# Kernel optimization log

Measured on AMD Instinct MI355X. Metric: run time of the kernel, lower is better.

Reference implementation:

```python
import jax, jax.numpy as jnp
import numpy as np

VOCAB = 32000   # vocab size
EDIM = 1024     # embedding dim
HDIM = 1024     # encoder hidden dim (fhid dim)
NACTS = 2       # ACTS = {'push': 0, 'pop': 1}
NCLASSES = 3
L = 256         # len_total
B = 128         # bsz
PAD = 0         # padding_idx
PUSH, POP = 0, 1


def setup_inputs() -> dict:
    key = jax.random.key(0)
    ks = jax.random.split(key, 10)

    def mk_seq(kt, kl):
        tok = jax.random.randint(kt, (L, B), 1, VOCAB)          # non-pad tokens
        lens = jax.random.randint(kl, (B,), L // 2, L - 1)      # ragged lengths
        t = jnp.arange(L)[:, None]
        # first lens+1 positions non-pad (so lens = L - n_pad - 1 as in the module)
        return jnp.where(t < lens[None, :] + 1, tok, PAD)

    seq1 = mk_seq(ks[0], ks[1])
    seq2 = mk_seq(ks[2], ks[3])

    def w(k, shp):
        return (jax.random.normal(k, shp, jnp.float32) * 0.02)

    return {
        "seq1": seq1, "seq2": seq2,
        "emb": w(ks[4], (VOCAB, EDIM)),
        "W_top": w(ks[5], (EDIM, HDIM)), "b_top": jnp.zeros((HDIM,), jnp.float32),
        "W_act": w(ks[6], (EDIM, NACTS)), "b_act": jnp.zeros((NACTS,), jnp.float32),
        "W1": w(ks[7], (4 * HDIM, HDIM)), "b1": jnp.zeros((HDIM,), jnp.float32),
        "W2": w(ks[8], (HDIM, NCLASSES)), "b2": jnp.zeros((NCLASSES,), jnp.float32),
    }


def _encode(seq, emb, W_top, b_top, W_act, b_act):
    # stub stack-encoder: time dim 2L-1 (one shift + one reduce step per token)
    seq_ext = jnp.concatenate([seq, seq[:-1]], axis=0)          # [2L-1, B]
    x = emb[seq_ext]                                            # [2L-1, B, E]
    top = jnp.tanh(jnp.einsum('tbe,eh->tbh', x, W_top) + b_top) # [2L-1, B, H]
    act = jax.nn.softmax(jnp.einsum('tbe,ea->tba', x, W_act) + b_act, axis=-1)
    return top, act


def _ragged_stats(act, Ts, bsz):
    # masked equivalents of the per-sample python loops over acts[:T, b, :]
    Tmax = act.shape[0]
    mask = (jnp.arange(Tmax)[:, None] < Ts[None, :]).astype(act.dtype)  # [2L-1, B]
    Tf = Ts.astype(act.dtype)
    push, pop = act[:, :, PUSH], act[:, :, POP]
    sum_push = (push * mask).sum(axis=0) / Tf                   # [B]
    sum_pop = ((pop * mask).sum(axis=0) + 1.0) / Tf             # [B]
    diff = jnp.sqrt((((push - pop) ** 2) * mask).sum(axis=0)) / Tf  # [B]
    dis = jnp.linalg.norm(sum_push - sum_pop) / bsz             # scalar
    return dis, diff.sum() / bsz


def reference(seq1, seq2, emb, W_top, b_top, W_act, b_act, W1, b1, W2, b2):
    bsz = seq1.shape[1]
    top1, act1 = _encode(seq1, emb, W_top, b_top, W_act, b_act)
    top2, act2 = _encode(seq2, emb, W_top, b_top, W_act, b_act)

    lens1 = seq1.shape[0] - (seq1 == PAD).sum(axis=0) - 1
    lens2 = seq2.shape[0] - (seq2 == PAD).sum(axis=0) - 1
    Ts1 = 2 * lens1 - 1
    Ts2 = 2 * lens2 - 1

    barange = jnp.arange(bsz)
    fhid1 = top1[Ts1 - 1, barange]                              # [B, H] ragged gather
    fhid2 = top2[Ts2 - 1, barange]

    u = jnp.concatenate([fhid1, fhid2, jnp.abs(fhid1 - fhid2), fhid1 * fhid2], axis=-1)
    res_clf = jax.nn.relu(u @ W1 + b1) @ W2 + b2                # [B, nclasses]

    dis1, diff1 = _ragged_stats(act1, Ts1, bsz)
    dis2, diff2 = _ragged_stats(act2, Ts2, bsz)
    return (res_clf, dis1, dis2, diff1, diff2)
```

## Files before the change

kernel.cpp:

```cpp
#include <hip/hip_runtime.h>
#include <math.h>

#define LL 256
#define BB 128
#define EDIM 1024
#define HDIM 1024
#define VOCAB 32000

#define NKSF 8
#define NKS  64

#define WS_EACT   0
#define WS_DELTA  32000
#define WS_DIFFB  32256
#define WS_FHID   33024
#define WS_BIG    295168

#define APAD 68

__device__ __forceinline__ void fma4(float4& a, float s, const float4& w) {
  a.x = fmaf(s, w.x, a.x); a.y = fmaf(s, w.y, a.y);
  a.z = fmaf(s, w.z, a.z); a.w = fmaf(s, w.w, a.w);
}

extern "C" __global__ __launch_bounds__(256)
void k_fh_eact(const float* __restrict__ emb, const float* __restrict__ Wtop,
               const float* __restrict__ Wact,
               const int* __restrict__ seq1, const int* __restrict__ seq2,
               float* __restrict__ fpart, float* __restrict__ Eact) {
  __shared__ float ash[128 * APAD];
  __shared__ int stok[128];
  int blk = blockIdx.x, tid = threadIdx.x;
  if (blk >= 256) {
    int lane = tid & 63, wave = tid >> 6;
    int v = (blk - 256) * 4 + wave;
    const float4* row = (const float4*)(emb + (size_t)v * EDIM);
    const float4* w4 = (const float4*)Wact;
    float a0 = 0.f;
#pragma unroll
    for (int it = 0; it < 4; ++it) {
      int i = lane + it * 64;
      float4 x = row[i];
      float4 wa = w4[2 * i];
      float4 wb = w4[2 * i + 1];
      a0 = fmaf(x.x, wa.x - wa.y, a0);
      a0 = fmaf(x.y, wa.z - wa.w, a0);
      a0 = fmaf(x.z, wb.x - wb.y, a0);
      a0 = fmaf(x.w, wb.z - wb.w, a0);
    }
#pragma unroll
    for (int off = 32; off; off >>= 1)
      a0 += __shfl_down(a0, off, 64);
    if (lane == 0) Eact[v] = a0;
    return;
  }
  int ks = blk >> 5, rb = (blk >> 4) & 1, cb = blk & 15;
  int cg = tid & 15, rgr = tid >> 4;
  int c0 = cb * 64 + cg * 4;
  int kbase = ks * 128;
  const int* seq = rb ? seq2 : seq1;
  {
    int c = tid >> 1, h = tid & 1;
    int z = 0;
    int base = h * 128;
    for (int r = 0; r < 128; ++r)
      z += (seq[(base + r) * BB + c] == 0) ? 1 : 0;
    z += __shfl_xor(z, 1, 64);
    if (h == 0) {
      int lens = 255 - z;
      int tt = 2 * lens - 2;
      int idx = (tt < LL) ? tt : tt - LL;
      stok[c] = seq[idx * BB + c];
    }
  }
  float4 acc[8];
#pragma unroll
  for (int r = 0; r < 8; ++r) acc[r] = make_float4(0.f, 0.f, 0.f, 0.f);
#pragma unroll
  for (int ch = 0; ch < 2; ++ch) {
    int kg = kbase + ch * 64;
    __syncthreads();
    for (int idx = tid; idx < 128 * 16; idx += 256) {
      int r = idx >> 4, q = idx & 15;
      *(float4*)&ash[r * APAD + q * 4] =
          ((const float4*)(emb + (size_t)stok[r] * EDIM + kg))[q];
    }
    __syncthreads();
    const float* Wp = Wtop + (size_t)kg * HDIM + c0;
    float4 w[4];
#pragma unroll
    for (int j = 0; j < 4; ++j) w[j] = *(const float4*)(Wp + (size_t)j * HDIM);
#pragma unroll
    for (int kk = 0; kk < 64; kk += 4) {
      float4 wn[4];
      if (kk + 4 < 64) {
#pragma unroll
        for (int j = 0; j < 4; ++j) wn[j] = *(const float4*)(Wp + (size_t)(kk + 4 + j) * HDIM);
      }
#pragma unroll
      for (int r = 0; r < 8; ++r) {
        float4 a = *(const float4*)&ash[(rgr * 8 + r) * APAD + kk];
        fma4(acc[r], a.x, w[0]); fma4(acc[r], a.y, w[1]);
        fma4(acc[r], a.z, w[2]); fma4(acc[r], a.w, w[3]);
      }
#pragma unroll
      for (int j = 0; j < 4; ++j) w[j] = wn[j];
    }
  }
  float* dst = fpart + ((size_t)ks * 256 + rb * 128 + rgr * 8) * HDIM + c0;
#pragma unroll
  for (int r = 0; r < 8; ++r)
    *(float4*)(dst + (size_t)r * HDIM) = acc[r];
}

extern "C" __global__ __launch_bounds__(256)
void k_ftanh_stats(const float* __restrict__ fpart, const float* __restrict__ btop,
                   const int* __restrict__ seq1, const int* __restrict__ seq2,
                   const float* __restrict__ Eact, const float* __restrict__ b_act,
                   float* __restrict__ fhid, float* __restrict__ delta,
                   float* __restrict__ diffb) {
  int blk = blockIdx.x, tid = threadIdx.x;
  if (blk < 256) {
    int g = blk * 256 + tid;
    float4 s = ((const float4*)fpart)[g];
#pragma unroll
    for (int k = 1; k < NKSF; ++k) {
      float4 p = ((const float4*)fpart)[(size_t)k * 65536 + g];
      s.x += p.x; s.y += p.y; s.z += p.z; s.w += p.w;
    }
    float4 b = ((const float4*)btop)[g & 255];
    ((float4*)fhid)[g] = make_float4(tanhf(s.x + b.x), tanhf(s.y + b.y),
                                     tanhf(s.z + b.z), tanhf(s.w + b.w));
    return;
  }
  int sb = blk - 256;
  int s = sb >> 7, b = sb & 127;
  const int* seq = s ? seq2 : seq1;
  __shared__ int col[LL];
  __shared__ int zred[256];
  __shared__ float redf[256];
  int v = seq[tid * BB + b];
  col[tid] = v;
  zred[tid] = (v == 0) ? 1 : 0;
  __syncthreads();
  for (int off = 128; off; off >>= 1) {
    if (tid < off) zred[tid] += zred[tid + off];
    __syncthreads();
  }
  int lens = LL - zred[0] - 1;
  int Ts = 2 * lens - 1;
  float ba = b_act[0] - b_act[1];
  float sp = 0.f, sq = 0.f;
  for (int t = tid; t < Ts; t += 256) {
    int tok = (t < LL) ? col[t] : col[t - LL];
    float d = Eact[tok] + ba;
    float p0 = 1.0f / (1.0f + expf(-d));
    float dd = 2.f * p0 - 1.f;
    sp += dd;
    sq = fmaf(dd, dd, sq);
  }
  redf[tid] = sp; __syncthreads();
  for (int off = 128; off; off >>= 1) { if (tid < off) redf[tid] += redf[tid + off]; __syncthreads(); }
  float tsp = redf[0]; __syncthreads();
  redf[tid] = sq; __syncthreads();
  for (int off = 128; off; off >>= 1) { if (tid < off) redf[tid] += redf[tid + off]; __syncthreads(); }
  if (tid == 0) {
    float Tf = (float)Ts;
    delta[sb] = (tsp - 1.0f) / Tf;
    diffb[sb] = sqrtf(redf[0]) / Tf;
  }
}

extern "C" __global__ __launch_bounds__(256)
void k_part(const float* __restrict__ fhid, const float* __restrict__ W1,
            float* __restrict__ part) {
  __shared__ float ush[128 * APAD];
  int blk = blockIdx.x, tid = threadIdx.x;
  int ksb = blk >> 4, cb = blk & 15;
  int cg = tid & 15, rgr = tid >> 4;
  int c0 = cb * 64 + cg * 4;
  int kbase = ksb * 64;
  int seg = kbase >> 10;
  int fb4 = (kbase & 1023) >> 2;
  const float4* f4 = (const float4*)fhid;
#pragma unroll
  for (int j = 0; j < 8; ++j) {
    int idx = tid + j * 256;
    int r = idx >> 4, q = idx & 15;
    float4 u;
    if (seg == 0) u = f4[r * 256 + fb4 + q];
    else if (seg == 1) u = f4[(128 + r) * 256 + fb4 + q];
    else {
      float4 f1 = f4[r * 256 + fb4 + q];
      float4 f2 = f4[(128 + r) * 256 + fb4 + q];
      if (seg == 2)
        u = make_float4(fabsf(f1.x - f2.x), fabsf(f1.y - f2.y),
                        fabsf(f1.z - f2.z), fabsf(f1.w - f2.w));
      else
        u = make_float4(f1.x * f2.x, f1.y * f2.y, f1.z * f2.z, f1.w * f2.w);
    }
    *(float4*)&ush[r * APAD + q * 4] = u;
  }
  float4 acc[8];
#pragma unroll
  for (int r = 0; r < 8; ++r) acc[r] = make_float4(0.f, 0.f, 0.f, 0.f);
  __syncthreads();
  const float* Wp = W1 + (size_t)kbase * HDIM + c0;
  float4 w[4];
#pragma unroll
  for (int j = 0; j < 4; ++j) w[j] = *(const float4*)(Wp + (size_t)j * HDIM);
#pragma unroll
  for (int kk = 0; kk < 64; kk += 4) {
    float4 wn[4];
    if (kk + 4 < 64) {
#pragma unroll
      for (int j = 0; j < 4; ++j) wn[j] = *(const float4*)(Wp + (size_t)(kk + 4 + j) * HDIM);
    }
#pragma unroll
    for (int r = 0; r < 8; ++r) {
      float4 a = *(const float4*)&ush[(rgr * 8 + r) * APAD + kk];
      fma4(acc[r], a.x, w[0]); fma4(acc[r], a.y, w[1]);
      fma4(acc[r], a.z, w[2]); fma4(acc[r], a.w, w[3]);
    }
#pragma unroll
    for (int j = 0; j < 4; ++j) w[j] = wn[j];
  }
  float* dst = part + ((size_t)ksb * 128 + rgr * 8) * HDIM + c0;
#pragma unroll
  for (int r = 0; r < 8; ++r)
    *(float4*)(dst + (size_t)r * HDIM) = acc[r];
}

extern "C" __global__ __launch_bounds__(256)
void k_clf_final(const float* __restrict__ part, const float* __restrict__ b1,
                 const float* __restrict__ W2, const float* __restrict__ b2,
                 const float* __restrict__ delta, const float* __restrict__ diffb,
                 float* __restrict__ out) {
  int blk = blockIdx.x, tid = threadIdx.x;
  __shared__ float red[768];
  if (blk == 128) {
    for (int s = 0; s < 2; ++s) {
      float v = 0.f, w = 0.f;
      if (tid < BB) { float d = delta[s * BB + tid]; v = d * d; w = diffb[s * BB + tid]; }
      red[tid] = v; __syncthreads();
      for (int off = 128; off; off >>= 1) { if (tid < off) red[tid] += red[tid + off]; __syncthreads(); }
      if (tid == 0) out[384 + s] = sqrtf(red[0]) / (float)BB;
      __syncthreads();
      red[tid] = w; __syncthreads();
      for (int off = 128; off; off >>= 1) { if (tid < off) red[tid] += red[tid + off]; __syncthreads(); }
      if (tid == 0) out[386 + s] = red[0] / (float)BB;
      __syncthreads();
    }
    return;
  }
  int b = blk;
  float4 p = ((const float4*)b1)[tid];
  const float4* p4 = (const float4*)part;
  for (int ks = 0; ks < NKS; ++ks) {
    float4 q = p4[((size_t)ks * 128 + b) * 256 + tid];
    p.x += q.x; p.y += q.y; p.z += q.z; p.w += q.w;
  }
  p.x = fmaxf(p.x, 0.f); p.y = fmaxf(p.y, 0.f);
  p.z = fmaxf(p.z, 0.f); p.w = fmaxf(p.w, 0.f);
  int k0 = tid * 4;
  float a0 = 0.f, a1 = 0.f, a2 = 0.f;
  a0 = fmaf(p.x, W2[(k0 + 0) * 3 + 0], a0); a1 = fmaf(p.x, W2[(k0 + 0) * 3 + 1], a1); a2 = fmaf(p.x, W2[(k0 + 0) * 3 + 2], a2);
  a0 = fmaf(p.y, W2[(k0 + 1) * 3 + 0], a0); a1 = fmaf(p.y, W2[(k0 + 1) * 3 + 1], a1); a2 = fmaf(p.y, W2[(k0 + 1) * 3 + 2], a2);
  a0 = fmaf(p.z, W2[(k0 + 2) * 3 + 0], a0); a1 = fmaf(p.z, W2[(k0 + 2) * 3 + 1], a1); a2 = fmaf(p.z, W2[(k0 + 2) * 3 + 2], a2);
  a0 = fmaf(p.w, W2[(k0 + 3) * 3 + 0], a0); a1 = fmaf(p.w, W2[(k0 + 3) * 3 + 1], a1); a2 = fmaf(p.w, W2[(k0 + 3) * 3 + 2], a2);
  red[tid] = a0; red[256 + tid] = a1; red[512 + tid] = a2;
  __syncthreads();
  for (int off = 128; off; off >>= 1) {
    if (tid < off) {
      red[tid] += red[tid + off];
      red[256 + tid] += red[256 + tid + off];
      red[512 + tid] += red[512 + tid + off];
    }
    __syncthreads();
  }
  if (tid == 0) {
    out[b * 3 + 0] = red[0]   + b2[0];
    out[b * 3 + 1] = red[256] + b2[1];
    out[b * 3 + 2] = red[512] + b2[2];
  }
}

extern "C" void kernel_launch(void* const* d_in, const int* in_sizes, int n_in,
                              void* d_out, int out_size, void* d_ws, size_t ws_size,
                              hipStream_t stream) {
  const int*   seq1  = (const int*)  d_in[0];
  const int*   seq2  = (const int*)  d_in[1];
  const float* emb   = (const float*)d_in[2];
  const float* W_top = (const float*)d_in[3];
  const float* b_top = (const float*)d_in[4];
  const float* W_act = (const float*)d_in[5];
  const float* b_act = (const float*)d_in[6];
  const float* W1    = (const float*)d_in[7];
  const float* b1    = (const float*)d_in[8];
  const float* W2    = (const float*)d_in[9];
  const float* b2    = (const float*)d_in[10];
  float* out = (float*)d_out;
  float* ws  = (float*)d_ws;

  float* Eact  = ws + WS_EACT;
  float* delta = ws + WS_DELTA;
  float* diffb = ws + WS_DIFFB;
  float* fhid  = ws + WS_FHID;
  float* bigb  = ws + WS_BIG;

  hipLaunchKernelGGL(k_fh_eact,     dim3(256 + 8000), dim3(256), 0, stream, emb, W_top, W_act, seq1, seq2, bigb, Eact);
  hipLaunchKernelGGL(k_ftanh_stats, dim3(512),        dim3(256), 0, stream, bigb, b_top, seq1, seq2, Eact, b_act, fhid, delta, diffb);
  hipLaunchKernelGGL(k_part,        dim3(1024),       dim3(256), 0, stream, fhid, W1, bigb);
  hipLaunchKernelGGL(k_clf_final,   dim3(129),        dim3(256), 0, stream, bigb, b1, W2, b2, delta, diffb, out);
}
```

Before: 259.7 us.

## Fuse four kernels into one cooperative persistent kernel with grid syncs

Replaces the four separate launches with a single 512-block cooperative kernel that uses grid-wide syncs between phases. It also repartitions the work: the W_top GEMM uses 128 blocks with a larger K split (4 splits instead of 8), the Eact pass becomes a grid-stride loop, and the W1 GEMM uses smaller M tiles with 16 K-splits instead of 64. The aim is to remove launch gaps and shrink the partial-sum traffic. The cost is fewer blocks doing the heavy first GEMM and the overhead of the grid barriers.

```diff
diff --git a/kernel.cpp b/kernel.cpp
--- a/kernel.cpp
+++ b/kernel.cpp
@@ -1,20 +1,22 @@
 #include <hip/hip_runtime.h>
+#include <hip/hip_cooperative_groups.h>
 #include <math.h>
 
 #define LL 256
 #define BB 128
 #define EDIM 1024
 #define HDIM 1024
-#define VOCAB 32000
-
-#define NKSF 8
-#define NKS  64
+
+#define NKSF 4
+#define NKS  16
+#define GRID 512
 
 #define WS_EACT   0
 #define WS_DELTA  32000
 #define WS_DIFFB  32256
 #define WS_FHID   33024
-#define WS_BIG    295168
+#define WS_FPART  295168
+#define WS_PART   (295168 + 1048576)
 
 #define APAD 68
 
@@ -23,103 +25,108 @@
   a.z = fmaf(s, w.z, a.z); a.w = fmaf(s, w.w, a.w);
 }
 
-extern "C" __global__ __launch_bounds__(256)
-void k_fh_eact(const float* __restrict__ emb, const float* __restrict__ Wtop,
-               const float* __restrict__ Wact,
-               const int* __restrict__ seq1, const int* __restrict__ seq2,
-               float* __restrict__ fpart, float* __restrict__ Eact) {
-  __shared__ float ash[128 * APAD];
+extern "C" __global__ __launch_bounds__(256, 4)
+void k_all(const float* __restrict__ emb, const float* __restrict__ Wtop,
+           const float* __restrict__ Wact, const int* __restrict__ seq1,
+           const int* __restrict__ seq2, const float* __restrict__ btop,
+           const float* __restrict__ bact, const float* __restrict__ W1,
+           const float* __restrict__ b1, const float* __restrict__ W2,
+           const float* __restrict__ b2, float* __restrict__ Eact,
+           float* __restrict__ fpart, float* __restrict__ fhid,
+           float* __restrict__ delta, float* __restrict__ diffb,
+           float* __restrict__ part, float* __restrict__ out) {
+  __shared__ float ash[64 * APAD];
   __shared__ int stok[128];
+  cooperative_groups::grid_group gg = cooperative_groups::this_grid();
   int blk = blockIdx.x, tid = threadIdx.x;
-  if (blk >= 256) {
-    int lane = tid & 63, wave = tid >> 6;
-    int v = (blk - 256) * 4 + wave;
-    const float4* row = (const float4*)(emb + (size_t)v * EDIM);
+  int lane = tid & 63, wave = tid >> 6;
+  int cgi = tid & 15, rgr = tid >> 4;
+
+  if (blk < 128) {
+    int ks = blk >> 5, rb = (blk >> 4) & 1, cb = blk & 15;
+    int c0 = cb * 64 + cgi * 4;
+    const int* seq = rb ? seq2 : seq1;
+    {
+      int c = tid >> 1, h = tid & 1;
+      int z = 0, base = h * 128;
+      for (int r = 0; r < 128; ++r)
+        z += (seq[(base + r) * BB + c] == 0) ? 1 : 0;
+      z += __shfl_xor(z, 1, 64);
+      if (h == 0) {
+        int lens = 255 - z;
+        int tt = 2 * lens - 2;
+        int idx = (tt < LL) ? tt : tt - LL;
+        stok[c] = seq[idx * BB + c];
+      }
+    }
+    for (int tch = 0; tch < 2; ++tch) {
+      int tr0 = tch * 64;
+      float4 acc[4];
+#pragma unroll
+      for (int r = 0; r < 4; ++r) acc[r] = make_float4(0.f, 0.f, 0.f, 0.f);
+      for (int kch = 0; kch < 4; ++kch) {
+        int kg = ks * 256 + kch * 64;
+        __syncthreads();
+#pragma unroll
+        for (int j = 0; j < 4; ++j) {
+          int idx = tid + j * 256;
+          int r = idx >> 4, q = idx & 15;
+          *(float4*)&ash[r * APAD + q * 4] =
+              ((const float4*)(emb + (size_t)stok[tr0 + r] * EDIM + kg))[q];
+        }
+        __syncthreads();
+        const float* Wp = Wtop + (size_t)kg * HDIM + c0;
+        float4 w[4];
+#pragma unroll
+        for (int j = 0; j < 4; ++j) w[j] = *(const float4*)(Wp + (size_t)j * HDIM);
+#pragma unroll
+        for (int kk = 0; kk < 64; kk += 4) {
+          float4 wn[4];
+          if (kk + 4 < 64) {
+#pragma unroll
+            for (int j = 0; j < 4; ++j)
+              wn[j] = *(const float4*)(Wp + (size_t)(kk + 4 + j) * HDIM);
+          }
+#pragma unroll
+          for (int r = 0; r < 4; ++r) {
+            float4 a = *(const float4*)&ash[(rgr * 4 + r) * APAD + kk];
+            fma4(acc[r], a.x, w[0]); fma4(acc[r], a.y, w[1]);
+            fma4(acc[r], a.z, w[2]); fma4(acc[r], a.w, w[3]);
+          }
+#pragma unroll
+          for (int j = 0; j < 4; ++j) w[j] = wn[j];
+        }
+      }
+      float* dst = fpart + ((size_t)ks * 256 + rb * 128 + tr0 + rgr * 4) * HDIM + c0;
+#pragma unroll
+      for (int r = 0; r < 4; ++r)
+        *(float4*)(dst + (size_t)r * HDIM) = acc[r];
+    }
+  } else {
+    int gw = (blk - 128) * 4 + wave;
     const float4* w4 = (const float4*)Wact;
-    float a0 = 0.f;
-#pragma unroll
-    for (int it = 0; it < 4; ++it) {
-      int i = lane + it * 64;
-      float4 x = row[i];
-      float4 wa = w4[2 * i];
-      float4 wb = w4[2 * i + 1];
-      a0 = fmaf(x.x, wa.x - wa.y, a0);
-      a0 = fmaf(x.y, wa.z - wa.w, a0);
-      a0 = fmaf(x.z, wb.x - wb.y, a0);
-      a0 = fmaf(x.w, wb.z - wb.w, a0);
-    }
-#pragma unroll
-    for (int off = 32; off; off >>= 1)
-      a0 += __shfl_down(a0, off, 64);
-    if (lane == 0) Eact[v] = a0;
-    return;
+    for (int v = gw; v < 32000; v += 1536) {
+      const float4* row = (const float4*)(emb + (size_t)v * EDIM);
+      float a0 = 0.f;
+#pragma unroll
+      for (int it = 0; it < 4; ++it) {
+        int i = lane + it * 64;
+        float4 x = row[i];
+        float4 wa = w4[2 * i];
+        float4 wb = w4[2 * i + 1];
+        a0 = fmaf(x.x, wa.x - wa.y, a0);
+        a0 = fmaf(x.y, wa.z - wa.w, a0);
+        a0 = fmaf(x.z, wb.x - wb.y, a0);
+        a0 = fmaf(x.w, wb.z - wb.w, a0);
+      }
+#pragma unroll
+      for (int off = 32; off; off >>= 1)
+        a0 += __shfl_down(a0, off, 64);
+      if (lane == 0) Eact[v] = a0;
+    }
   }
-  int ks = blk >> 5, rb = (blk >> 4) & 1, cb = blk & 15;
-  int cg = tid & 15, rgr = tid >> 4;
-  int c0 = cb * 64 + cg * 4;
-  int kbase = ks * 128;
-  const int* seq = rb ? seq2 : seq1;
-  {
-    int c = tid >> 1, h = tid & 1;
-    int z = 0;
-    int base = h * 128;
-    for (int r = 0; r < 128; ++r)
-      z += (seq[(base + r) * BB + c] == 0) ? 1 : 0;
-    z += __shfl_xor(z, 1, 64);
-    if (h == 0) {
-      int lens = 255 - z;
-      int tt = 2 * lens - 2;
-      int idx = (tt < LL) ? tt : tt - LL;
-      stok[c] = seq[idx * BB + c];
-    }
-  }
-  float4 acc[8];
-#pragma unroll
-  for (int r = 0; r < 8; ++r) acc[r] = make_float4(0.f, 0.f, 0.f, 0.f);
-#pragma unroll
-  for (int ch = 0; ch < 2; ++ch) {
-    int kg = kbase + ch * 64;
-    __syncthreads();
-    for (int idx = tid; idx < 128 * 16; idx += 256) {
-      int r = idx >> 4, q = idx & 15;
-      *(float4*)&ash[r * APAD + q * 4] =
-          ((const float4*)(emb + (size_t)stok[r] * EDIM + kg))[q];
-    }
-    __syncthreads();
-    const float* Wp = Wtop + (size_t)kg * HDIM + c0;
-    float4 w[4];
-#pragma unroll
-    for (int j = 0; j < 4; ++j) w[j] = *(const float4*)(Wp + (size_t)j * HDIM);
-#pragma unroll
-    for (int kk = 0; kk < 64; kk += 4) {
-      float4 wn[4];
-      if (kk + 4 < 64) {
-#pragma unroll
-        for (int j = 0; j < 4; ++j) wn[j] = *(const float4*)(Wp + (size_t)(kk + 4 + j) * HDIM);
-      }
-#pragma unroll
-      for (int r = 0; r < 8; ++r) {
-        float4 a = *(const float4*)&ash[(rgr * 8 + r) * APAD + kk];
-        fma4(acc[r], a.x, w[0]); fma4(acc[r], a.y, w[1]);
-        fma4(acc[r], a.z, w[2]); fma4(acc[r], a.w, w[3]);
-      }
-#pragma unroll
-      for (int j = 0; j < 4; ++j) w[j] = wn[j];
-    }
-  }
-  float* dst = fpart + ((size_t)ks * 256 + rb * 128 + rgr * 8) * HDIM + c0;
-#pragma unroll
-  for (int r = 0; r < 8; ++r)
-    *(float4*)(dst + (size_t)r * HDIM) = acc[r];
-}
-
-extern "C" __global__ __launch_bounds__(256)
-void k_ftanh_stats(const float* __restrict__ fpart, const float* __restrict__ btop,
-                   const int* __restrict__ seq1, const int* __restrict__ seq2,
-                   const float* __restrict__ Eact, const float* __restrict__ b_act,
-                   float* __restrict__ fhid, float* __restrict__ delta,
-                   float* __restrict__ diffb) {
-  int blk = blockIdx.x, tid = threadIdx.x;
+  gg.sync();
+
   if (blk < 256) {
     int g = blk * 256 + tid;
     float4 s = ((const float4*)fpart)[g];
@@ -131,114 +138,145 @@
     float4 b = ((const float4*)btop)[g & 255];
     ((float4*)fhid)[g] = make_float4(tanhf(s.x + b.x), tanhf(s.y + b.y),
                                      tanhf(s.z + b.z), tanhf(s.w + b.w));
-    return;
+  } else {
+    int sb = blk - 256;
+    int s = sb >> 7, b = sb & 127;
+    const int* seq = s ? seq2 : seq1;
+    int* col = (int*)ash;
+    int* zred = col + 256;
+    float* redf = (float*)(zred + 256);
+    int v = seq[tid * BB + b];
+    col[tid] = v;
+    zred[tid] = (v == 0) ? 1 : 0;
+    __syncthreads();
+    for (int off = 128; off; off >>= 1) {
+      if (tid < off) zred[tid] += zred[tid + off];
+      __syncthreads();
+    }
+    int lens = LL - zred[0] - 1;
+    int Ts = 2 * lens - 1;
+    float ba = bact[0] - bact[1];
+    float sp = 0.f, sq = 0.f;
+    for (int t = tid; t < Ts; t += 256) {
+      int tok = (t < LL) ? col[t] : col[t - LL];
+      float d = Eact[tok] + ba;
+      float p0 = 1.0f / (1.0f + expf(-d));
+      float dd = 2.f * p0 - 1.f;
+      sp += dd;
+      sq = fmaf(dd, dd, sq);
+    }
+    redf[tid] = sp; __syncthreads();
+    for (int off = 128; off; off >>= 1) { if (tid < off) redf[tid] += redf[tid + off]; __syncthreads(); }
+    float tsp = redf[0]; __syncthreads();
+    redf[tid] = sq; __syncthreads();
+    for (int off = 128; off; off >>= 1) { if (tid < off) redf[tid] += redf[tid + off]; __syncthreads(); }
+    if (tid == 0) {
+      float Tf = (float)Ts;
+      delta[sb] = (tsp - 1.0f) / Tf;
+      diffb[sb] = sqrtf(redf[0]) / Tf;
+    }
   }
-  int sb = blk - 256;
-  int s = sb >> 7, b = sb & 127;
-  const int* seq = s ? seq2 : seq1;
-  __shared__ int col[LL];
-  __shared__ int zred[256];
-  __shared__ float redf[256];
-  int v = seq[tid * BB + b];
-  col[tid] = v;
-  zred[tid] = (v == 0) ? 1 : 0;
-  __syncthreads();
-  for (int off = 128; off; off >>= 1) {
-    if (tid < off) zred[tid] += zred[tid + off];
+  gg.sync();
+
+  {
+    const float4* f4 = (const float4*)fhid;
+    for (int u = blk; u < 1024; u += GRID) {
+      int ksb = u >> 6, mb = (u >> 4) & 3, cbu = u & 15;
+      int c0 = cbu * 64 + cgi * 4;
+      int m0 = mb * 32;
+      float4 acc[2];
+      acc[0] = make_float4(0.f, 0.f, 0.f, 0.f);
+      acc[1] = make_float4(0.f, 0.f, 0.f, 0.f);
+      for (int kch = 0; kch < 4; ++kch) {
+        int kg = ksb * 256 + kch * 64;
+        int seg = kg >> 10;
+        int fb4 = (kg & 1023) >> 2;
+        __syncthreads();
+#pragma unroll
+        for (int j = 0; j < 2; ++j) {
+          int idx = tid + j * 256;
+          int r = idx >> 4, q = idx & 15;
+          int row = m0 + r;
+          float4 uv;
+          if (seg == 0) uv = f4[row * 256 + fb4 + q];
+          else if (seg == 1) uv = f4[(128 + row) * 256 + fb4 + q];
+          else {
+            float4 f1v = f4[row * 256 + fb4 + q];
+            float4 f2v = f4[(128 + row) * 256 + fb4 + q];
+            if (seg == 2)
+              uv = make_float4(fabsf(f1v.x - f2v.x), fabsf(f1v.y - f2v.y),
+                               fabsf(f1v.z - f2v.z), fabsf(f1v.w - f2v.w));
+            else
+              uv = make_float4(f1v.x * f2v.x, f1v.y * f2v.y,
+                               f1v.z * f2v.z, f1v.w * f2v.w);
+          }
+          *(float4*)&ash[r * APAD + q * 4] = uv;
+        }
+        __syncthreads();
+        const float* Wp = W1 + (size_t)kg * HDIM + c0;
+        float4 w[4];
+#pragma unroll
+        for (int j = 0; j < 4; ++j) w[j] = *(const float4*)(Wp + (size_t)j * HDIM);
+#pragma unroll
+        for (int kk = 0; kk < 64; kk += 4) {
+          float4 wn[4];
+          if (kk + 4 < 64) {
+#pragma unroll
+            for (int j = 0; j < 4; ++j)
+              wn[j] = *(const float4*)(Wp + (size_t)(kk + 4 + j) * HDIM);
+          }
+#pragma unroll
+          for (int r = 0; r < 2; ++r) {
+            float4 a = *(const float4*)&ash[(rgr * 2 + r) * APAD + kk];
+            fma4(acc[r], a.x, w[0]); fma4(acc[r], a.y, w[1]);
+            fma4(acc[r], a.z, w[2]); fma4(acc[r], a.w, w[3]);
+          }
+#pragma unroll
+          for (int j = 0; j < 4; ++j) w[j] = wn[j];
+        }
+      }
+      float* dst = part + ((size_t)ksb * 128 + m0 + rgr * 2) * HDIM + c0;
+      *(float4*)dst = acc[0];
+      *(float4*)(dst + HDIM) = acc[1];
+    }
+  }
+  gg.sync();
+
+  if (blk < 128) {
+    int b = blk;
+    float* red = ash;
+    float4 p = ((const float4*)b1)[tid];
+    const float4* p4 = (const float4*)part;
+#pragma unroll
+    for (int ksi = 0; ksi < NKS; ++ksi) {
+      float4 q = p4[((size_t)ksi * 128 + b) * 256 + tid];
+      p.x += q.x; p.y += q.y; p.z += q.z; p.w += q.w;
+    }
+    p.x = fmaxf(p.x, 0.f); p.y = fmaxf(p.y, 0.f);
+    p.z = fmaxf(p.z, 0.f); p.w = fmaxf(p.w, 0.f);
+    int k0 = tid * 4;
+    float a0 = 0.f, a1 = 0.f, a2 = 0.f;
+    a0 = fmaf(p.x, W2[(k0 + 0) * 3 + 0], a0); a1 = fmaf(p.x, W2[(k0 + 0) * 3 + 1], a1); a2 = fmaf(p.x, W2[(k0 + 0) * 3 + 2], a2);
+    a0 = fmaf(p.y, W2[(k0 + 1) * 3 + 0], a0); a1 = fmaf(p.y, W2[(k0 + 1) * 3 + 1], a1); a2 = fmaf(p.y, W2[(k0 + 1) * 3 + 2], a2);
+    a0 = fmaf(p.z, W2[(k0 + 2) * 3 + 0], a0); a1 = fmaf(p.z, W2[(k0 + 2) * 3 + 1], a1); a2 = fmaf(p.z, W2[(k0 + 2) * 3 + 2], a2);
+    a0 = fmaf(p.w, W2[(k0 + 3) * 3 + 0], a0); a1 = fmaf(p.w, W2[(k0 + 3) * 3 + 1], a1); a2 = fmaf(p.w, W2[(k0 + 3) * 3 + 2], a2);
+    red[tid] = a0; red[256 + tid] = a1; red[512 + tid] = a2;
     __syncthreads();
-  }
-  int lens = LL - zred[0] - 1;
-  int Ts = 2 * lens - 1;
-  float ba = b_act[0] - b_act[1];
-  float sp = 0.f, sq = 0.f;
-  for (int t = tid; t < Ts; t += 256) {
-    int tok = (t < LL) ? col[t] : col[t - LL];
-    float d = Eact[tok] + ba;
-    float p0 = 1.0f / (1.0f + expf(-d));
-    float dd = 2.f * p0 - 1.f;
-    sp += dd;
-    sq = fmaf(dd, dd, sq);
-  }
-  redf[tid] = sp; __syncthreads();
-  for (int off = 128; off; off >>= 1) { if (tid < off) redf[tid] += redf[tid + off]; __syncthreads(); }
-  float tsp = redf[0]; __syncthreads();
-  redf[tid] = sq; __syncthreads();
-  for (int off = 128; off; off >>= 1) { if (tid < off) redf[tid] += redf[tid + off]; __syncthreads(); }
-  if (tid == 0) {
-    float Tf = (float)Ts;
-    delta[sb] = (tsp - 1.0f) / Tf;
-    diffb[sb] = sqrtf(redf[0]) / Tf;
-  }
-}
-
-extern "C" __global__ __launch_bounds__(256)
-void k_part(const float* __restrict__ fhid, const float* __restrict__ W1,
-            float* __restrict__ part) {
-  __shared__ float ush[128 * APAD];
-  int blk = blockIdx.x, tid = threadIdx.x;
-  int ksb = blk >> 4, cb = blk & 15;
-  int cg = tid & 15, rgr = tid >> 4;
-  int c0 = cb * 64 + cg * 4;
-  int kbase = ksb * 64;
-  int seg = kbase >> 10;
-  int fb4 = (kbase & 1023) >> 2;
-  const float4* f4 = (const float4*)fhid;
-#pragma unroll
-  for (int j = 0; j < 8; ++j) {
-    int idx = tid + j * 256;
-    int r = idx >> 4, q = idx & 15;
-    float4 u;
-    if (seg == 0) u = f4[r * 256 + fb4 + q];
-    else if (seg == 1) u = f4[(128 + r) * 256 + fb4 + q];
-    else {
-      float4 f1 = f4[r * 256 + fb4 + q];
-      float4 f2 = f4[(128 + r) * 256 + fb4 + q];
-      if (seg == 2)
-        u = make_float4(fabsf(f1.x - f2.x), fabsf(f1.y - f2.y),
-                        fabsf(f1.z - f2.z), fabsf(f1.w - f2.w));
-      else
-        u = make_float4(f1.x * f2.x, f1.y * f2.y, f1.z * f2.z, f1.w * f2.w);
-    }
-    *(float4*)&ush[r * APAD + q * 4] = u;
-  }
-  float4 acc[8];
-#pragma unroll
-  for (int r = 0; r < 8; ++r) acc[r] = make_float4(0.f, 0.f, 0.f, 0.f);
-  __syncthreads();
-  const float* Wp = W1 + (size_t)kbase * HDIM + c0;
-  float4 w[4];
-#pragma unroll
-  for (int j = 0; j < 4; ++j) w[j] = *(const float4*)(Wp + (size_t)j * HDIM);
-#pragma unroll
-  for (int kk = 0; kk < 64; kk += 4) {
-    float4 wn[4];
-    if (kk + 4 < 64) {
-#pragma unroll
-      for (int j = 0; j < 4; ++j) wn[j] = *(const float4*)(Wp + (size_t)(kk + 4 + j) * HDIM);
-    }
-#pragma unroll
-    for (int r = 0; r < 8; ++r) {
-      float4 a = *(const float4*)&ush[(rgr * 8 + r) * APAD + kk];
-      fma4(acc[r], a.x, w[0]); fma4(acc[r], a.y, w[1]);
-      fma4(acc[r], a.z, w[2]); fma4(acc[r], a.w, w[3]);
-    }
-#pragma unroll
-    for (int j = 0; j < 4; ++j) w[j] = wn[j];
-  }
-  float* dst = part + ((size_t)ksb * 128 + rgr * 8) * HDIM + c0;
-#pragma unroll
-  for (int r = 0; r < 8; ++r)
-    *(float4*)(dst + (size_t)r * HDIM) = acc[r];
-}
-
-extern "C" __global__ __launch_bounds__(256)
-void k_clf_final(const float* __restrict__ part, const float* __restrict__ b1,
-                 const float* __restrict__ W2, const float* __restrict__ b2,
-                 const float* __restrict__ delta, const float* __restrict__ diffb,
-                 float* __restrict__ out) {
-  int blk = blockIdx.x, tid = threadIdx.x;
-  __shared__ float red[768];
-  if (blk == 128) {
+    for (int off = 128; off; off >>= 1) {
+      if (tid < off) {
+        red[tid] += red[tid + off];
+        red[256 + tid] += red[256 + tid + off];
+        red[512 + tid] += red[512 + tid + off];
+      }
+      __syncthreads();
+    }
+    if (tid == 0) {
+      out[b * 3 + 0] = red[0]   + b2[0];
+      out[b * 3 + 1] = red[256] + b2[1];
+      out[b * 3 + 2] = red[512] + b2[2];
+    }
+  } else if (blk == 128) {
+    float* red = ash;
     for (int s = 0; s < 2; ++s) {
       float v = 0.f, w = 0.f;
       if (tid < BB) { float d = delta[s * BB + tid]; v = d * d; w = diffb[s * BB + tid]; }
@@ -251,37 +289,6 @@
       if (tid == 0) out[386 + s] = red[0] / (float)BB;
       __syncthreads();
     }
-    return;
-  }
-  int b = blk;
-  float4 p = ((const float4*)b1)[tid];
-  const float4* p4 = (const float4*)part;
-  for (int ks = 0; ks < NKS; ++ks) {
-    float4 q = p4[((size_t)ks * 128 + b) * 256 + tid];
-    p.x += q.x; p.y += q.y; p.z += q.z; p.w += q.w;
-  }
-  p.x = fmaxf(p.x, 0.f); p.y = fmaxf(p.y, 0.f);
-  p.z = fmaxf(p.z, 0.f); p.w = fmaxf(p.w, 0.f);
-  int k0 = tid * 4;
-  float a0 = 0.f, a1 = 0.f, a2 = 0.f;
-  a0 = fmaf(p.x, W2[(k0 + 0) * 3 + 0], a0); a1 = fmaf(p.x, W2[(k0 + 0) * 3 + 1], a1); a2 = fmaf(p.x, W2[(k0 + 0) * 3 + 2], a2);
-  a0 = fmaf(p.y, W2[(k0 + 1) * 3 + 0], a0); a1 = fmaf(p.y, W2[(k0 + 1) * 3 + 1], a1); a2 = fmaf(p.y, W2[(k0 + 1) * 3 + 2], a2);
-  a0 = fmaf(p.z, W2[(k0 + 2) * 3 + 0], a0); a1 = fmaf(p.z, W2[(k0 + 2) * 3 + 1], a1); a2 = fmaf(p.z, W2[(k0 + 2) * 3 + 2], a2);
-  a0 = fmaf(p.w, W2[(k0 + 3) * 3 + 0], a0); a1 = fmaf(p.w, W2[(k0 + 3) * 3 + 1], a1); a2 = fmaf(p.w, W2[(k0 + 3) * 3 + 2], a2);
-  red[tid] = a0; red[256 + tid] = a1; red[512 + tid] = a2;
-  __syncthreads();
-  for (int off = 128; off; off >>= 1) {
-    if (tid < off) {
-      red[tid] += red[tid + off];
-      red[256 + tid] += red[256 + tid + off];
-      red[512 + tid] += red[512 + tid + off];
-    }
-    __syncthreads();
-  }
-  if (tid == 0) {
-    out[b * 3 + 0] = red[0]   + b2[0];
-    out[b * 3 + 1] = red[256] + b2[1];
-    out[b * 3 + 2] = red[512] + b2[2];
   }
 }
 
@@ -306,10 +313,14 @@
   float* delta = ws + WS_DELTA;
   float* diffb = ws + WS_DIFFB;
   float* fhid  = ws + WS_FHID;
-  float* bigb  = ws + WS_BIG;
-
-  hipLaunchKernelGGL(k_fh_eact,     dim3(256 + 8000), dim3(256), 0, stream, emb, W_top, W_act, seq1, seq2, bigb, Eact);
-  hipLaunchKernelGGL(k_ftanh_stats, dim3(512),        dim3(256), 0, stream, bigb, b_top, seq1, seq2, Eact, b_act, fhid, delta, diffb);
-  hipLaunchKernelGGL(k_part,        dim3(1024),       dim3(256), 0, stream, fhid, W1, bigb);
-  hipLaunchKernelGGL(k_clf_final,   dim3(129),        dim3(256), 0, stream, bigb, b1, W2, b2, delta, diffb, out);
+  float* fpart = ws + WS_FPART;
+  float* part  = ws + WS_PART;
+
+  void* args[] = { (void*)&emb, (void*)&W_top, (void*)&W_act, (void*)&seq1,
+                   (void*)&seq2, (void*)&b_top, (void*)&b_act, (void*)&W1,
+                   (void*)&b1, (void*)&W2, (void*)&b2, (void*)&Eact,
+                   (void*)&fpart, (void*)&fhid, (void*)&delta, (void*)&diffb,
+                   (void*)&part, (void*)&out };
+  hipLaunchCooperativeKernel((const void*)k_all, dim3(GRID), dim3(256),
+                             args, 0, stream);
 }
```

Result: slower. 543.5 us (+109.2%).

## Rebalance W1 GEMM split-K: fewer K splits, M-blocked tiles, smaller partials

Applied to the files above, without the earlier changes.

Splits the classifier's first GEMM into 32-row M blocks, each looping over four 64-wide K chunks, and cuts the split-K factor from 64 to 16. The partial-sum buffer written by k_part and then read by k_clf_final becomes four times smaller, and the reduction loop is unrolled. In exchange, each W1 tile is now read by four M blocks instead of one, so W1 traffic goes up unless the cache absorbs it. The shared-memory row pad also changes to 66 floats, which leaves the float4 LDS accesses unaligned on odd rows.

```diff
diff --git a/kernel.cpp b/kernel.cpp
--- a/kernel.cpp
+++ b/kernel.cpp
@@ -8,7 +8,7 @@
 #define VOCAB 32000
 
 #define NKSF 8
-#define NKS  64
+#define NKS  16
 
 #define WS_EACT   0
 #define WS_DELTA  32000
@@ -16,7 +16,7 @@
 #define WS_FHID   33024
 #define WS_BIG    295168
 
-#define APAD 68
+#define APAD 66
 
 __device__ __forceinline__ void fma4(float4& a, float s, const float4& w) {
   a.x = fmaf(s, w.x, a.x); a.y = fmaf(s, w.y, a.y);
@@ -174,61 +174,67 @@
 extern "C" __global__ __launch_bounds__(256)
 void k_part(const float* __restrict__ fhid, const float* __restrict__ W1,
             float* __restrict__ part) {
-  __shared__ float ush[128 * APAD];
+  __shared__ float ush[32 * APAD];
   int blk = blockIdx.x, tid = threadIdx.x;
-  int ksb = blk >> 4, cb = blk & 15;
+  int ksb = blk >> 6, mb = (blk >> 4) & 3, cb = blk & 15;
   int cg = tid & 15, rgr = tid >> 4;
   int c0 = cb * 64 + cg * 4;
-  int kbase = ksb * 64;
-  int seg = kbase >> 10;
-  int fb4 = (kbase & 1023) >> 2;
+  int m0 = mb * 32;
   const float4* f4 = (const float4*)fhid;
-#pragma unroll
-  for (int j = 0; j < 8; ++j) {
-    int idx = tid + j * 256;
-    int r = idx >> 4, q = idx & 15;
-    float4 u;
-    if (seg == 0) u = f4[r * 256 + fb4 + q];
-    else if (seg == 1) u = f4[(128 + r) * 256 + fb4 + q];
-    else {
-      float4 f1 = f4[r * 256 + fb4 + q];
-      float4 f2 = f4[(128 + r) * 256 + fb4 + q];
-      if (seg == 2)
-        u = make_float4(fabsf(f1.x - f2.x), fabsf(f1.y - f2.y),
-                        fabsf(f1.z - f2.z), fabsf(f1.w - f2.w));
-      else
-        u = make_float4(f1.x * f2.x, f1.y * f2.y, f1.z * f2.z, f1.w * f2.w);
-    }
-    *(float4*)&ush[r * APAD + q * 4] = u;
-  }
-  float4 acc[8];
-#pragma unroll
-  for (int r = 0; r < 8; ++r) acc[r] = make_float4(0.f, 0.f, 0.f, 0.f);
-  __syncthreads();
-  const float* Wp = W1 + (size_t)kbase * HDIM + c0;
-  float4 w[4];
-#pragma unroll
-  for (int j = 0; j < 4; ++j) w[j] = *(const float4*)(Wp + (size_t)j * HDIM);
-#pragma unroll
-  for (int kk = 0; kk < 64; kk += 4) {
-    float4 wn[4];
-    if (kk + 4 < 64) {
-#pragma unroll
-      for (int j = 0; j < 4; ++j) wn[j] = *(const float4*)(Wp + (size_t)(kk + 4 + j) * HDIM);
-    }
-#pragma unroll
-    for (int r = 0; r < 8; ++r) {
-      float4 a = *(const float4*)&ush[(rgr * 8 + r) * APAD + kk];
-      fma4(acc[r], a.x, w[0]); fma4(acc[r], a.y, w[1]);
-      fma4(acc[r], a.z, w[2]); fma4(acc[r], a.w, w[3]);
-    }
-#pragma unroll
-    for (int j = 0; j < 4; ++j) w[j] = wn[j];
-  }
-  float* dst = part + ((size_t)ksb * 128 + rgr * 8) * HDIM + c0;
-#pragma unroll
-  for (int r = 0; r < 8; ++r)
-    *(float4*)(dst + (size_t)r * HDIM) = acc[r];
+  float4 acc[2];
+  acc[0] = make_float4(0.f, 0.f, 0.f, 0.f);
+  acc[1] = make_float4(0.f, 0.f, 0.f, 0.f);
+  for (int kch = 0; kch < 4; ++kch) {
+    int kg = ksb * 256 + kch * 64;
+    int seg = kg >> 10;
+    int fb4 = (kg & 1023) >> 2;
+    __syncthreads();
+#pragma unroll
+    for (int j = 0; j < 2; ++j) {
+      int idx = tid + j * 256;
+      int r = idx >> 4, q = idx & 15;
+      int row = m0 + r;
+      float4 uv;
+      if (seg == 0) uv = f4[row * 256 + fb4 + q];
+      else if (seg == 1) uv = f4[(128 + row) * 256 + fb4 + q];
+      else {
+        float4 f1v = f4[row * 256 + fb4 + q];
+        float4 f2v = f4[(128 + row) * 256 + fb4 + q];
+        if (seg == 2)
+          uv = make_float4(fabsf(f1v.x - f2v.x), fabsf(f1v.y - f2v.y),
+                           fabsf(f1v.z - f2v.z), fabsf(f1v.w - f2v.w));
+        else
+          uv = make_float4(f1v.x * f2v.x, f1v.y * f2v.y,
+                           f1v.z * f2v.z, f1v.w * f2v.w);
+      }
+      *(float4*)&ush[r * APAD + q * 4] = uv;
+    }
+    __syncthreads();
+    const float* Wp = W1 + (size_t)kg * HDIM + c0;
+    float4 w[4];
+#pragma unroll
+    for (int j = 0; j < 4; ++j) w[j] = *(const float4*)(Wp + (size_t)j * HDIM);
+#pragma unroll
+    for (int kk = 0; kk < 64; kk += 4) {
+      float4 wn[4];
+      if (kk + 4 < 64) {
+#pragma unroll
+        for (int j = 0; j < 4; ++j)
+          wn[j] = *(const float4*)(Wp + (size_t)(kk + 4 + j) * HDIM);
+      }
+#pragma unroll
+      for (int r = 0; r < 2; ++r) {
+        float4 a = *(const float4*)&ush[(rgr * 2 + r) * APAD + kk];
+        fma4(acc[r], a.x, w[0]); fma4(acc[r], a.y, w[1]);
+        fma4(acc[r], a.z, w[2]); fma4(acc[r], a.w, w[3]);
+      }
+#pragma unroll
+      for (int j = 0; j < 4; ++j) w[j] = wn[j];
+    }
+  }
+  float* dst = part + ((size_t)ksb * 128 + m0 + rgr * 2) * HDIM + c0;
+  *(float4*)dst = acc[0];
+  *(float4*)(dst + HDIM) = acc[1];
 }
 
 extern "C" __global__ __launch_bounds__(256)
@@ -256,6 +262,7 @@
   int b = blk;
   float4 p = ((const float4*)b1)[tid];
   const float4* p4 = (const float4*)part;
+#pragma unroll
   for (int ks = 0; ks < NKS; ++ks) {
     float4 q = p4[((size_t)ks * 128 + b) * 256 + tid];
     p.x += q.x; p.y += q.y; p.z += q.z; p.w += q.w;
```

Measured after the change: 270.2 us. 4.0% more time.
